# Optimization experiments

Hardware: AMD Instinct MI355X
Metric: run time of the kernel (lower is better)

## Reference

```python
import jax, jax.numpy as jnp
import numpy as np

NUM_BRANCHES = 3
NUM_LAYERS = 4
HIDDEN = 256
IN_DIM = 128
NUM_GRAPHS = 256
NUM_CLASSES = 10
TOPK_RATIO = 0.5
GATE_INIT = 0.8


def matrix_neighbors(branch, layer, num_branches):
    nbrs = []
    if layer > 0:
        nbrs.append((branch, layer - 1))
    for other in (branch - 1, branch + 1):
        if 0 <= other < num_branches:
            nbrs.append((other, layer))
    if layer > 0:
        for other in (branch - 1, branch + 1):
            if 0 <= other < num_branches:
                nbrs.append((other, layer - 1))
    return nbrs


def topk_mask(t, ratio):
    d = t.shape[-1]
    k = max(1, min(d, int(np.ceil(d * ratio))))
    if k >= d:
        return jnp.ones_like(t)
    _, idx = jax.lax.top_k(jnp.abs(t), k)
    rows = jnp.arange(t.shape[0])[:, None]
    return jnp.zeros_like(t).at[rows, idx].set(1.0)


def setup_inputs():
    key = jax.random.key(0)
    ks = jax.random.split(key, 10)
    n, e = 50000, 800000
    x = jax.random.normal(ks[0], (n, IN_DIM), dtype=jnp.float32)
    edge_index = jax.random.randint(ks[1], (2, e), 0, n)
    batch = jnp.sort(jax.random.randint(ks[2], (n,), 0, NUM_GRAPHS))
    s = 0.05
    Win = jax.random.normal(ks[3], (NUM_BRANCHES, IN_DIM, HIDDEN), dtype=jnp.float32) * s
    b_in = jnp.zeros((NUM_BRANCHES, HIDDEN), dtype=jnp.float32)
    Whid = jax.random.normal(ks[4], (NUM_LAYERS - 1, NUM_BRANCHES, HIDDEN, HIDDEN), dtype=jnp.float32) * s
    bhid = jnp.zeros((NUM_LAYERS - 1, NUM_BRANCHES, HIDDEN), dtype=jnp.float32)
    gate_logit = jnp.asarray(np.log(GATE_INIT / (1.0 - GATE_INIT)), dtype=jnp.float32)
    Wc = jax.random.normal(ks[5], (HIDDEN, NUM_CLASSES), dtype=jnp.float32) * s
    bc = jnp.zeros((NUM_CLASSES,), dtype=jnp.float32)
    return {"x": x, "edge_index": edge_index, "batch": batch, "Win": Win,
            "b_in": b_in, "Whid": Whid, "bhid": bhid, "gate_logit": gate_logit,
            "Wc": Wc, "bc": bc}


def _forward(x, edge_index, batch, Win, b_in, Whid, bhid, gate_logit, Wc, bc):
    n = x.shape[0]
    loops = jnp.arange(n)
    row = jnp.concatenate([edge_index[0], loops])  # source
    col = jnp.concatenate([edge_index[1], loops])  # target
    deg = jax.ops.segment_sum(jnp.ones_like(col, dtype=x.dtype), col, num_segments=n)
    dinv = jnp.where(deg > 0, jax.lax.rsqrt(deg), 0.0)
    norm = dinv[row] * dinv[col]  # [E+N]

    def gcn(h, W, b):
        hw = h @ W  # [n, H]
        agg = jax.ops.segment_sum(hw[row] * norm[:, None], col, num_segments=n)
        return agg + b

    gate = jax.nn.sigmoid(gate_logit)
    states = [x for _ in range(NUM_BRANCHES)]
    for layer in range(NUM_LAYERS):
        props = []
        for b in range(NUM_BRANCHES):
            if layer == 0:
                p = gcn(states[b], Win[b], b_in[b])
            else:
                p = gcn(states[b], Whid[layer - 1, b], bhid[layer - 1, b])
            props.append(jax.nn.relu(p))
        new_states = []
        for b in range(NUM_BRANCHES):
            fused = props[b]
            nbrs = matrix_neighbors(b, layer, NUM_BRANCHES)
            if nbrs:
                rs = jnp.zeros_like(fused)
                for (sb, sl) in nbrs:
                    src = props[sb] if sl == layer else states[sb]
                    rs = rs + src * topk_mask(src, TOPK_RATIO)
                fused = fused + gate * rs
            new_states.append(jax.nn.relu(fused))  # dropout is identity in eval
        states = new_states

    counts = jax.ops.segment_sum(jnp.ones((n,), dtype=x.dtype), batch, num_segments=NUM_GRAPHS)
    denom = jnp.maximum(counts, 1.0)[:, None]
    embs = [jax.ops.segment_sum(s, batch, num_segments=NUM_GRAPHS) / denom for s in states]
    final = jnp.mean(jnp.stack(embs, axis=0), axis=0)  # [G, H]
    logits = final @ Wc + bc
    return logits, final


def reference(x, edge_index, batch, Win, b_in, Whid, bhid, gate_logit, Wc, bc):
    return _forward(x, edge_index, batch, Win, b_in, Whid, bhid, gate_logit, Wc, bc)
```

## Files before the change

### kernel.cpp

```cpp
#include <hip/hip_runtime.h>
#include <hip/hip_fp16.h>

#define NB 3
#define HIDDEN 256
#define INDIM 128
#define NGRAPH 256
#define NCLS 10
#define NMAX 50048
#define EMAX 800000

typedef unsigned short u16;
typedef unsigned long long ull;
typedef _Float16 f16_t;
typedef f16_t f16x8 __attribute__((ext_vector_type(8)));
typedef float f32x4 __attribute__((ext_vector_type(4)));

__device__ __align__(16) u16   g_states[(size_t)NB * NMAX * HIDDEN];
__device__ __align__(16) u16   g_props [(size_t)NB * NMAX * HIDDEN];
__device__ __align__(16) u16   g_agg3 [(size_t)NB * NMAX * HIDDEN];
__device__ __align__(16) u16   g_xh    [(size_t)NMAX * INDIM];
__device__ __align__(16) u16   g_whin [(size_t)NB * INDIM * HIDDEN];
__device__ __align__(16) u16   g_whid [(size_t)9 * HIDDEN * HIDDEN];
__device__ float g_fin   [NGRAPH * HIDDEN];
__device__ float g_dinv  [NMAX];
__device__ float g_ewts  [EMAX];
__device__ int   g_rowptr[NMAX + 1];
__device__ int   g_cidx  [EMAX];
__device__ int   g_cnt   [NMAX];
__device__ int   g_gs    [NGRAPH];
__device__ int   g_gc    [NGRAPH];

union HU { u16 u; __half h; };
__device__ __forceinline__ float h2f(u16 v) { HU x; x.u = v; return __half2float(x.h); }
__device__ __forceinline__ u16 f2h(float f) { HU x; x.h = __float2half_rn(f); return x.u; }
__device__ __forceinline__ float relu_f(float x) { return x > 0.f ? x : 0.f; }

__device__ __forceinline__ void fma8(float* acc, uint4 v, float w) {
    unsigned uu[4] = {v.x, v.y, v.z, v.w};
    #pragma unroll
    for (int q = 0; q < 4; ++q) {
        HU lo, hi; lo.u = (u16)(uu[q] & 0xFFFFu); hi.u = (u16)(uu[q] >> 16);
        acc[q * 2 + 0] += w * __half2float(lo.h);
        acc[q * 2 + 1] += w * __half2float(hi.h);
    }
}

__global__ void zero_cnt_k(int n) {
    int i = blockIdx.x * 256 + threadIdx.x;
    if (i < n) g_cnt[i] = 0;
}
__global__ void zero_gk() {
    int i = threadIdx.x;
    g_gs[i] = 0; g_gc[i] = 0;
}
__global__ void cvt_xh_k(const float* __restrict__ x, int cnt) {
    int i = blockIdx.x * 256 + threadIdx.x;
    if (i < cnt) g_xh[i] = f2h(x[i]);
}
__global__ void cvt_wt_k(const float* __restrict__ src, int which, int K, int total) {
    int i = blockIdx.x * 256 + threadIdx.x;
    if (i >= total) return;
    int kc = K * 256;
    int b = i / kc; int rem = i - b * kc;
    int k = rem >> 8; int c = rem & 255;
    u16* dst = which ? g_whid : g_whin;
    dst[(size_t)b * kc + (size_t)c * K + k] = f2h(src[i]);
}

__global__ void count_edges_k(const int* __restrict__ col, int E) {
    int i = blockIdx.x * 256 + threadIdx.x;
    if (i < E) atomicAdd(&g_cnt[col[i]], 1);
}
__global__ void dinv_k(int n) {
    int i = blockIdx.x * 256 + threadIdx.x;
    if (i < n) g_dinv[i] = rsqrtf((float)(g_cnt[i] + 1));
}
__global__ __launch_bounds__(1024) void scan_k(int n) {
    __shared__ int sm[1024];
    __shared__ int carry_s;
    int t = threadIdx.x;
    if (t == 0) carry_s = 0;
    __syncthreads();
    for (int base = 0; base < n; base += 1024) {
        int i = base + t;
        int v = (i < n) ? g_cnt[i] : 0;
        sm[t] = v;
        __syncthreads();
        for (int off = 1; off < 1024; off <<= 1) {
            int u = (t >= off) ? sm[t - off] : 0;
            __syncthreads();
            sm[t] += u;
            __syncthreads();
        }
        int incl = sm[t];
        int c0 = carry_s;
        if (i < n) g_rowptr[i] = c0 + incl - v;
        __syncthreads();
        if (t == 0) carry_s += sm[1023];
        __syncthreads();
    }
    if (t == 0) g_rowptr[n] = carry_s;
}
__global__ void fill_csr_k(const int* __restrict__ row, const int* __restrict__ col, int E) {
    int i = blockIdx.x * 256 + threadIdx.x;
    if (i >= E) return;
    int r = row[i], c = col[i];
    int pos = g_rowptr[c] + atomicAdd(&g_cnt[c], 1);
    g_cidx[pos] = r;
    g_ewts[pos] = g_dinv[r] * g_dinv[c];
}

__global__ __launch_bounds__(256) void agg256x3_k(int n) {
    int node = blockIdx.x * 4 + (threadIdx.x >> 6);
    if (node >= n) return;
    int lane = threadIdx.x & 63;
    int half = lane >> 5;
    int li   = lane & 31;
    size_t pstride = (size_t)n * 32;
    const uint4* Sv = (const uint4*)g_states;
    float acc0[8] = {0,0,0,0,0,0,0,0}, acc1[8] = {0,0,0,0,0,0,0,0}, acc2[8] = {0,0,0,0,0,0,0,0};
    int e0 = g_rowptr[node], deg = g_rowptr[node + 1] - e0;
    int m = deg + 1;
    int j = half;
    if (half == 0) {
        float di = g_dinv[node];
        float w0 = di * di;
        size_t base = (size_t)node * 32 + li;
        fma8(acc0, Sv[base], w0);
        fma8(acc1, Sv[base + pstride], w0);
        fma8(acc2, Sv[base + 2 * pstride], w0);
        j = 2;
    }
    #pragma unroll 2
    for (; j < m; j += 2) {
        int s = g_cidx[e0 + j - 1];
        float w = g_ewts[e0 + j - 1];
        size_t base = (size_t)s * 32 + li;
        uint4 v0 = Sv[base], v1 = Sv[base + pstride], v2 = Sv[base + 2 * pstride];
        fma8(acc0, v0, w); fma8(acc1, v1, w); fma8(acc2, v2, w);
    }
    #pragma unroll
    for (int q = 0; q < 8; ++q) {
        acc0[q] += __shfl_xor(acc0[q], 32);
        acc1[q] += __shfl_xor(acc1[q], 32);
        acc2[q] += __shfl_xor(acc2[q], 32);
    }
    if (half == 0) {
        size_t stA = (size_t)NMAX * 32;
        uint4* Av = (uint4*)g_agg3;
        uint4 o;
        unsigned* ou = (unsigned*)&o;
        #pragma unroll
        for (int q = 0; q < 4; ++q) ou[q] = (unsigned)f2h(acc0[q*2]) | ((unsigned)f2h(acc0[q*2+1]) << 16);
        Av[(size_t)node * 32 + li] = o;
        #pragma unroll
        for (int q = 0; q < 4; ++q) ou[q] = (unsigned)f2h(acc1[q*2]) | ((unsigned)f2h(acc1[q*2+1]) << 16);
        Av[(size_t)node * 32 + li + stA] = o;
        #pragma unroll
        for (int q = 0; q < 4; ++q) ou[q] = (unsigned)f2h(acc2[q*2]) | ((unsigned)f2h(acc2[q*2+1]) << 16);
        Av[(size_t)node * 32 + li + 2 * stA] = o;
    }
}

__global__ __launch_bounds__(256) void agg128_k(int n) {
    int node = blockIdx.x * 4 + (threadIdx.x >> 6);
    if (node >= n) return;
    int lane = threadIdx.x & 63;
    int grp = lane >> 4;
    int li  = lane & 15;
    const uint4* Xv = (const uint4*)g_xh;
    float acc[8] = {0,0,0,0,0,0,0,0};
    int e0 = g_rowptr[node], deg = g_rowptr[node + 1] - e0;
    int m = deg + 1;
    int j = grp;
    if (grp == 0) {
        float di = g_dinv[node];
        fma8(acc, Xv[(size_t)node * 16 + li], di * di);
        j = 4;
    }
    #pragma unroll 2
    for (; j < m; j += 4) {
        int s = g_cidx[e0 + j - 1];
        float w = g_ewts[e0 + j - 1];
        fma8(acc, Xv[(size_t)s * 16 + li], w);
    }
    #pragma unroll
    for (int q = 0; q < 8; ++q) {
        acc[q] += __shfl_xor(acc[q], 16);
        acc[q] += __shfl_xor(acc[q], 32);
    }
    if (grp == 0) {
        uint4 o; unsigned* ou = (unsigned*)&o;
        #pragma unroll
        for (int q = 0; q < 4; ++q) ou[q] = (unsigned)f2h(acc[q*2]) | ((unsigned)f2h(acc[q*2+1]) << 16);
        ((uint4*)g_agg3)[(size_t)node * 16 + li] = o;
    }
}

template<int K>
__global__ __launch_bounds__(256) void gemm_mfma_k(int wsel, size_t aStride,
        const float* __restrict__ bias0, int n) {
    int br = blockIdx.y;
    const f16_t* A  = (const f16_t*)g_agg3 + (size_t)br * aStride;
    const f16_t* Wt = (wsel < 0) ? (const f16_t*)g_whin + (size_t)br * K * 256
                                 : (const f16_t*)g_whid + (size_t)(wsel + br) * K * 256;
    const float* bias = bias0 + (size_t)br * 256;
    u16* C = g_props + (size_t)br * n * 256;
    int t = threadIdx.x, l = t & 63, w = t >> 6;
    int row0 = blockIdx.x * 64;
    int c0 = w * 64;
    int mrow = l & 15;
    int kg = (l >> 4) * 8;
    f32x4 acc[4][4];
    #pragma unroll
    for (int rt = 0; rt < 4; ++rt)
        #pragma unroll
        for (int ct = 0; ct < 4; ++ct) acc[rt][ct] = (f32x4){0.f, 0.f, 0.f, 0.f};

    for (int k0 = 0; k0 < K; k0 += 32) {
        f16x8 af[4], bf[4];
        #pragma unroll
        for (int rt = 0; rt < 4; ++rt) {
            int r = row0 + rt * 16 + mrow;
            af[rt] = *(const f16x8*)(A + (size_t)r * K + k0 + kg);
        }
        #pragma unroll
        for (int ct = 0; ct < 4; ++ct) {
            int c = c0 + ct * 16 + mrow;
            bf[ct] = *(const f16x8*)(Wt + (size_t)c * K + k0 + kg);
        }
        #pragma unroll
        for (int rt = 0; rt < 4; ++rt)
            #pragma unroll
            for (int ct = 0; ct < 4; ++ct)
                acc[rt][ct] = __builtin_amdgcn_mfma_f32_16x16x32_f16(af[rt], bf[ct], acc[rt][ct], 0, 0, 0);
    }
    int rb = (l >> 4) * 4;
    #pragma unroll
    for (int ct = 0; ct < 4; ++ct) {
        int c = c0 + ct * 16 + mrow;
        float bv = bias[c];
        #pragma unroll
        for (int rt = 0; rt < 4; ++rt) {
            #pragma unroll
            for (int q = 0; q < 4; ++q) {
                int r = row0 + rt * 16 + rb + q;
                if (r < n) C[(size_t)r * 256 + c] = f2h(relu_f(acc[rt][ct][q] + bv));
            }
        }
    }
}

template<int CNT>
__device__ __forceinline__ void topk_multi(const ushort4* hu, const float4* v, float4* out) {
    int lane = threadIdx.x & 63;
    unsigned lo[CNT], hi[CNT]; int cge[CNT];
    #pragma unroll
    for (int s = 0; s < CNT; ++s) { lo[s] = 0; hi[s] = 0x7BFF; cge[s] = 256; }
    for (int it = 0; it < 15; ++it) {
        #pragma unroll
        for (int s = 0; s < CNT; ++s) {
            unsigned mid = (lo[s] + hi[s] + 1) >> 1;
            int c = __popcll(__ballot(hu[s].x >= mid)) + __popcll(__ballot(hu[s].y >= mid))
                  + __popcll(__ballot(hu[s].z >= mid)) + __popcll(__ballot(hu[s].w >= mid));
            if (c >= 128) { lo[s] = mid; cge[s] = c; } else hi[s] = mid - 1;
        }
    }
    #pragma unroll
    for (int s = 0; s < CNT; ++s) {
        unsigned thr = lo[s];
        unsigned a0 = hu[s].x, a1 = hu[s].y, a2 = hu[s].z, a3 = hu[s].w;
        float4 r;
        if (cge[s] == 128) {
            r.x = (a0 >= thr) ? v[s].x : 0.f;
            r.y = (a1 >= thr) ? v[s].y : 0.f;
            r.z = (a2 >= thr) ? v[s].z : 0.f;
            r.w = (a3 >= thr) ? v[s].w : 0.f;
        } else {
            ull b0 = __ballot(a0 == thr), b1 = __ballot(a1 == thr);
            ull b2 = __ballot(a2 == thr), b3 = __ballot(a3 == thr);
            int cgt = __popcll(__ballot(a0 > thr)) + __popcll(__ballot(a1 > thr))
                    + __popcll(__ballot(a2 > thr)) + __popcll(__ballot(a3 > thr));
            int need = 128 - cgt;
            ull below = (lane == 0) ? 0ull : (~0ull >> (64 - lane));
            int base = __popcll(b0 & below) + __popcll(b1 & below)
                     + __popcll(b2 & below) + __popcll(b3 & below);
            int o0 = (int)((b0 >> lane) & 1), o1 = (int)((b1 >> lane) & 1), o2 = (int)((b2 >> lane) & 1);
            int p0 = base, p1 = base + o0, p2 = p1 + o1, p3 = p2 + o2;
            r.x = (a0 > thr || (a0 == thr && p0 < need)) ? v[s].x : 0.f;
            r.y = (a1 > thr || (a1 == thr && p1 < need)) ? v[s].y : 0.f;
            r.z = (a2 > thr || (a2 == thr && p2 < need)) ? v[s].z : 0.f;
            r.w = (a3 > thr || (a3 == thr && p3 < need)) ? v[s].w : 0.f;
        }
        out[s] = r;
    }
}

__device__ __forceinline__ float4 dec4(ushort4 h) {
    float4 r; r.x = h2f(h.x); r.y = h2f(h.y); r.z = h2f(h.z); r.w = h2f(h.w);
    return r;
}
__device__ __forceinline__ void st4h(u16* p, size_t off, float4 v) {
    ushort4 o; o.x = f2h(v.x); o.y = f2h(v.y); o.z = f2h(v.z); o.w = f2h(v.w);
    ((ushort4*)p)[off] = o;
}

__global__ __launch_bounds__(256) void fuse0_k(const float* __restrict__ gate_logit, int n) {
    int node = blockIdx.x * 4 + (threadIdx.x >> 6);
    if (node >= n) return;
    int lane = threadIdx.x & 63;
    size_t stride = (size_t)n * 64;
    size_t off = (size_t)node * 64 + lane;
    float g = 1.f / (1.f + expf(-gate_logit[0]));
    const ushort4* P = (const ushort4*)g_props;
    ushort4 hu[3]; float4 v[3], m[3];
    hu[0] = P[off]; hu[1] = P[off + stride]; hu[2] = P[off + 2 * stride];
    v[0] = dec4(hu[0]); v[1] = dec4(hu[1]); v[2] = dec4(hu[2]);
    topk_multi<3>(hu, v, m);
    float4 o0, o1, o2;
    o0.x = relu_f(v[0].x + g * m[1].x); o0.y = relu_f(v[0].y + g * m[1].y);
    o0.z = relu_f(v[0].z + g * m[1].z); o0.w = relu_f(v[0].w + g * m[1].w);
    o1.x = relu_f(v[1].x + g * (m[0].x + m[2].x)); o1.y = relu_f(v[1].y + g * (m[0].y + m[2].y));
    o1.z = relu_f(v[1].z + g * (m[0].z + m[2].z)); o1.w = relu_f(v[1].w + g * (m[0].w + m[2].w));
    o2.x = relu_f(v[2].x + g * m[1].x); o2.y = relu_f(v[2].y + g * m[1].y);
    o2.z = relu_f(v[2].z + g * m[1].z); o2.w = relu_f(v[2].w + g * m[1].w);
    st4h(g_states, off, o0); st4h(g_states, off + stride, o1); st4h(g_states, off + 2 * stride, o2);
}

__global__ __launch_bounds__(256) void fuse_k(const float* __restrict__ gate_logit, int n) {
    int node = blockIdx.x * 4 + (threadIdx.x >> 6);
    if (node >= n) return;
    int lane = threadIdx.x & 63;
    size_t stride = (size_t)n * 64;
    size_t off = (size_t)node * 64 + lane;
    float g = 1.f / (1.f + expf(-gate_logit[0]));
    const ushort4* P = (const ushort4*)g_props;
    const ushort4* S = (const ushort4*)g_states;
    ushort4 hu[6]; float4 v[6], m[6];
    hu[0] = P[off]; hu[1] = P[off + stride]; hu[2] = P[off + 2 * stride];
    hu[3] = S[off]; hu[4] = S[off + stride]; hu[5] = S[off + 2 * stride];
    #pragma unroll
    for (int s = 0; s < 6; ++s) v[s] = dec4(hu[s]);
    topk_multi<6>(hu, v, m);
    float4 o0, o1, o2;
    o0.x = relu_f(v[0].x + g * (m[3].x + m[1].x + m[4].x));
    o0.y = relu_f(v[0].y + g * (m[3].y + m[1].y + m[4].y));
    o0.z = relu_f(v[0].z + g * (m[3].z + m[1].z + m[4].z));
    o0.w = relu_f(v[0].w + g * (m[3].w + m[1].w + m[4].w));
    o1.x = relu_f(v[1].x + g * (m[4].x + m[0].x + m[3].x + m[2].x + m[5].x));
    o1.y = relu_f(v[1].y + g * (m[4].y + m[0].y + m[3].y + m[2].y + m[5].y));
    o1.z = relu_f(v[1].z + g * (m[4].z + m[0].z + m[3].z + m[2].z + m[5].z));
    o1.w = relu_f(v[1].w + g * (m[4].w + m[0].w + m[3].w + m[2].w + m[5].w));
    o2.x = relu_f(v[2].x + g * (m[5].x + m[1].x + m[4].x));
    o2.y = relu_f(v[2].y + g * (m[5].y + m[1].y + m[4].y));
    o2.z = relu_f(v[2].z + g * (m[5].z + m[1].z + m[4].z));
    o2.w = relu_f(v[2].w + g * (m[5].w + m[1].w + m[4].w));
    st4h(g_states, off, o0); st4h(g_states, off + stride, o1); st4h(g_states, off + 2 * stride, o2);
}

__global__ void gbounds_k(const int* __restrict__ batch, int n) {
    int i = blockIdx.x * 256 + threadIdx.x;
    if (i >= n) return;
    int g = batch[i];
    atomicAdd(&g_gc[g], 1);
    if (i == 0 || batch[i - 1] != g) g_gs[g] = i;
}

__global__ __launch_bounds__(256) void greduce_k(float* __restrict__ outfin, int n) {
    int g = blockIdx.x, d = threadIdx.x;
    size_t stride = (size_t)n * 256;
    int st = g_gs[g], c = g_gc[g];
    float a = 0.f;
    for (int i = st; i < st + c; ++i) {
        size_t o = (size_t)i * 256 + d;
        a += h2f(g_states[o]) + h2f(g_states[o + stride]) + h2f(g_states[o + 2 * stride]);
    }
    float r = a / (3.0f * (float)(c > 0 ? c : 1));
    g_fin[g * 256 + d] = r;
    outfin[(size_t)g * 256 + d] = r;
}

__global__ void logits_k(const float* __restrict__ Wc, const float* __restrict__ bc,
                         float* __restrict__ out) {
    int idx = blockIdx.x * 256 + threadIdx.x;
    if (idx >= NGRAPH * NCLS) return;
    int g = idx / NCLS, c = idx % NCLS;
    float s = bc[c];
    for (int k = 0; k < 256; ++k) s += g_fin[g * 256 + k] * Wc[k * NCLS + c];
    out[idx] = s;
}

extern "C" void kernel_launch(void* const* d_in, const int* in_sizes, int n_in,
                              void* d_out, int out_size, void* d_ws, size_t ws_size,
                              hipStream_t stream) {
    const float* x       = (const float*)d_in[0];
    const int*   eidx    = (const int*)d_in[1];
    const int*   batch   = (const int*)d_in[2];
    const float* Win     = (const float*)d_in[3];
    const float* b_in    = (const float*)d_in[4];
    const float* Whid    = (const float*)d_in[5];
    const float* bhid    = (const float*)d_in[6];
    const float* gate_l  = (const float*)d_in[7];
    const float* Wc      = (const float*)d_in[8];
    const float* bc      = (const float*)d_in[9];
    float* out = (float*)d_out;

    const int n = in_sizes[0] / INDIM;
    const int E = in_sizes[1] / 2;
    if (n > NMAX || E > EMAX) return;
    const int* erow = eidx;
    const int* ecol = eidx + E;

    float* outfin = out + NGRAPH * NCLS;

    const int TB = 256;
    dim3 b256(TB);
    int nblkN = (n + TB - 1) / TB;
    int eblk  = (E + TB - 1) / TB;
    int nblk4 = (n + 3) / 4;
    dim3 ggrid((n + 63) / 64, NB);

    zero_cnt_k<<<nblkN, b256, 0, stream>>>(n);
    cvt_xh_k<<<(n * INDIM + TB - 1) / TB, b256, 0, stream>>>(x, n * INDIM);
    cvt_wt_k<<<(NB * INDIM * HIDDEN + TB - 1) / TB, b256, 0, stream>>>(Win, 0, INDIM, NB * INDIM * HIDDEN);
    cvt_wt_k<<<(9 * HIDDEN * HIDDEN + TB - 1) / TB, b256, 0, stream>>>(Whid, 1, HIDDEN, 9 * HIDDEN * HIDDEN);
    count_edges_k<<<eblk, b256, 0, stream>>>(ecol, E);
    dinv_k<<<nblkN, b256, 0, stream>>>(n);
    scan_k<<<1, 1024, 0, stream>>>(n);
    zero_cnt_k<<<nblkN, b256, 0, stream>>>(n);
    fill_csr_k<<<eblk, b256, 0, stream>>>(erow, ecol, E);

    agg128_k<<<nblk4, b256, 0, stream>>>(n);
    gemm_mfma_k<INDIM><<<ggrid, b256, 0, stream>>>(-1, (size_t)0, b_in, n);
    fuse0_k<<<nblk4, b256, 0, stream>>>(gate_l, n);

    for (int l = 1; l < 4; ++l) {
        agg256x3_k<<<nblk4, b256, 0, stream>>>(n);
        gemm_mfma_k<HIDDEN><<<ggrid, b256, 0, stream>>>((l - 1) * NB, (size_t)NMAX * 256,
                bhid + (size_t)(l - 1) * NB * HIDDEN, n);
        fuse_k<<<nblk4, b256, 0, stream>>>(gate_l, n);
    }

    zero_gk<<<1, 256, 0, stream>>>();
    gbounds_k<<<nblkN, b256, 0, stream>>>(batch, n);
    greduce_k<<<NGRAPH, b256, 0, stream>>>(outfin, n);
    logits_k<<<(NGRAPH * NCLS + TB - 1) / TB, b256, 0, stream>>>(Wc, bc, out);
}
```

Measured before the change: 1.912 ms.

## Interleave branch states per node in node-major layout

```diff
diff --git a/kernel.cpp b/kernel.cpp
--- a/kernel.cpp
+++ b/kernel.cpp
@@ -15,9 +15,9 @@
 typedef f16_t f16x8 __attribute__((ext_vector_type(8)));
 typedef float f32x4 __attribute__((ext_vector_type(4)));
 
-__device__ __align__(16) u16   g_states[(size_t)NB * NMAX * HIDDEN];
-__device__ __align__(16) u16   g_props [(size_t)NB * NMAX * HIDDEN];
-__device__ __align__(16) u16   g_agg3 [(size_t)NB * NMAX * HIDDEN];
+__device__ __align__(16) u16   g_states[(size_t)NMAX * NB * HIDDEN];
+__device__ __align__(16) u16   g_props [(size_t)NMAX * NB * HIDDEN];
+__device__ __align__(16) u16   g_agg3 [(size_t)NMAX * NB * HIDDEN];
 __device__ __align__(16) u16   g_xh    [(size_t)NMAX * INDIM];
 __device__ __align__(16) u16   g_whin [(size_t)NB * INDIM * HIDDEN];
 __device__ __align__(16) u16   g_whid [(size_t)9 * HIDDEN * HIDDEN];
@@ -116,7 +116,6 @@
     int lane = threadIdx.x & 63;
     int half = lane >> 5;
     int li   = lane & 31;
-    size_t pstride = (size_t)n * 32;
     const uint4* Sv = (const uint4*)g_states;
     float acc0[8] = {0,0,0,0,0,0,0,0}, acc1[8] = {0,0,0,0,0,0,0,0}, acc2[8] = {0,0,0,0,0,0,0,0};
     int e0 = g_rowptr[node], deg = g_rowptr[node + 1] - e0;
@@ -125,18 +124,18 @@
     if (half == 0) {
         float di = g_dinv[node];
         float w0 = di * di;
-        size_t base = (size_t)node * 32 + li;
+        size_t base = (size_t)node * 96 + li;
         fma8(acc0, Sv[base], w0);
-        fma8(acc1, Sv[base + pstride], w0);
-        fma8(acc2, Sv[base + 2 * pstride], w0);
+        fma8(acc1, Sv[base + 32], w0);
+        fma8(acc2, Sv[base + 64], w0);
         j = 2;
     }
     #pragma unroll 2
     for (; j < m; j += 2) {
         int s = g_cidx[e0 + j - 1];
         float w = g_ewts[e0 + j - 1];
-        size_t base = (size_t)s * 32 + li;
-        uint4 v0 = Sv[base], v1 = Sv[base + pstride], v2 = Sv[base + 2 * pstride];
+        size_t base = (size_t)s * 96 + li;
+        uint4 v0 = Sv[base], v1 = Sv[base + 32], v2 = Sv[base + 64];
         fma8(acc0, v0, w); fma8(acc1, v1, w); fma8(acc2, v2, w);
     }
     #pragma unroll
@@ -146,19 +145,19 @@
         acc2[q] += __shfl_xor(acc2[q], 32);
     }
     if (half == 0) {
-        size_t stA = (size_t)NMAX * 32;
         uint4* Av = (uint4*)g_agg3;
+        size_t base = (size_t)node * 96 + li;
         uint4 o;
         unsigned* ou = (unsigned*)&o;
         #pragma unroll
         for (int q = 0; q < 4; ++q) ou[q] = (unsigned)f2h(acc0[q*2]) | ((unsigned)f2h(acc0[q*2+1]) << 16);
-        Av[(size_t)node * 32 + li] = o;
+        Av[base] = o;
         #pragma unroll
         for (int q = 0; q < 4; ++q) ou[q] = (unsigned)f2h(acc1[q*2]) | ((unsigned)f2h(acc1[q*2+1]) << 16);
-        Av[(size_t)node * 32 + li + stA] = o;
+        Av[base + 32] = o;
         #pragma unroll
         for (int q = 0; q < 4; ++q) ou[q] = (unsigned)f2h(acc2[q*2]) | ((unsigned)f2h(acc2[q*2+1]) << 16);
-        Av[(size_t)node * 32 + li + 2 * stA] = o;
+        Av[base + 64] = o;
     }
 }
 
@@ -198,14 +197,14 @@
 }
 
 template<int K>
-__global__ __launch_bounds__(256) void gemm_mfma_k(int wsel, size_t aStride,
+__global__ __launch_bounds__(256) void gemm_mfma_k(int wsel, int rowStride, int brMul,
         const float* __restrict__ bias0, int n) {
     int br = blockIdx.y;
-    const f16_t* A  = (const f16_t*)g_agg3 + (size_t)br * aStride;
+    const f16_t* A  = (const f16_t*)g_agg3 + (size_t)br * brMul;
     const f16_t* Wt = (wsel < 0) ? (const f16_t*)g_whin + (size_t)br * K * 256
                                  : (const f16_t*)g_whid + (size_t)(wsel + br) * K * 256;
     const float* bias = bias0 + (size_t)br * 256;
-    u16* C = g_props + (size_t)br * n * 256;
+    u16* C = g_props + (size_t)br * 256;
     int t = threadIdx.x, l = t & 63, w = t >> 6;
     int row0 = blockIdx.x * 64;
     int c0 = w * 64;
@@ -222,7 +221,7 @@
         #pragma unroll
         for (int rt = 0; rt < 4; ++rt) {
             int r = row0 + rt * 16 + mrow;
-            af[rt] = *(const f16x8*)(A + (size_t)r * K + k0 + kg);
+            af[rt] = *(const f16x8*)(A + (size_t)r * rowStride + k0 + kg);
         }
         #pragma unroll
         for (int ct = 0; ct < 4; ++ct) {
@@ -245,7 +244,7 @@
             #pragma unroll
             for (int q = 0; q < 4; ++q) {
                 int r = row0 + rt * 16 + rb + q;
-                if (r < n) C[(size_t)r * 256 + c] = f2h(relu_f(acc[rt][ct][q] + bv));
+                if (r < n) C[(size_t)r * 768 + c] = f2h(relu_f(acc[rt][ct][q] + bv));
             }
         }
     }
@@ -309,12 +308,11 @@
     int node = blockIdx.x * 4 + (threadIdx.x >> 6);
     if (node >= n) return;
     int lane = threadIdx.x & 63;
-    size_t stride = (size_t)n * 64;
-    size_t off = (size_t)node * 64 + lane;
+    size_t base4 = (size_t)node * 192 + lane;
     float g = 1.f / (1.f + expf(-gate_logit[0]));
     const ushort4* P = (const ushort4*)g_props;
     ushort4 hu[3]; float4 v[3], m[3];
-    hu[0] = P[off]; hu[1] = P[off + stride]; hu[2] = P[off + 2 * stride];
+    hu[0] = P[base4]; hu[1] = P[base4 + 64]; hu[2] = P[base4 + 128];
     v[0] = dec4(hu[0]); v[1] = dec4(hu[1]); v[2] = dec4(hu[2]);
     topk_multi<3>(hu, v, m);
     float4 o0, o1, o2;
@@ -324,21 +322,20 @@
     o1.z = relu_f(v[1].z + g * (m[0].z + m[2].z)); o1.w = relu_f(v[1].w + g * (m[0].w + m[2].w));
     o2.x = relu_f(v[2].x + g * m[1].x); o2.y = relu_f(v[2].y + g * m[1].y);
     o2.z = relu_f(v[2].z + g * m[1].z); o2.w = relu_f(v[2].w + g * m[1].w);
-    st4h(g_states, off, o0); st4h(g_states, off + stride, o1); st4h(g_states, off + 2 * stride, o2);
+    st4h(g_states, base4, o0); st4h(g_states, base4 + 64, o1); st4h(g_states, base4 + 128, o2);
 }
 
 __global__ __launch_bounds__(256) void fuse_k(const float* __restrict__ gate_logit, int n) {
     int node = blockIdx.x * 4 + (threadIdx.x >> 6);
     if (node >= n) return;
     int lane = threadIdx.x & 63;
-    size_t stride = (size_t)n * 64;
-    size_t off = (size_t)node * 64 + lane;
+    size_t base4 = (size_t)node * 192 + lane;
     float g = 1.f / (1.f + expf(-gate_logit[0]));
     const ushort4* P = (const ushort4*)g_props;
     const ushort4* S = (const ushort4*)g_states;
     ushort4 hu[6]; float4 v[6], m[6];
-    hu[0] = P[off]; hu[1] = P[off + stride]; hu[2] = P[off + 2 * stride];
-    hu[3] = S[off]; hu[4] = S[off + stride]; hu[5] = S[off + 2 * stride];
+    hu[0] = P[base4]; hu[1] = P[base4 + 64]; hu[2] = P[base4 + 128];
+    hu[3] = S[base4]; hu[4] = S[base4 + 64]; hu[5] = S[base4 + 128];
     #pragma unroll
     for (int s = 0; s < 6; ++s) v[s] = dec4(hu[s]);
     topk_multi<6>(hu, v, m);
@@ -355,7 +352,7 @@
     o2.y = relu_f(v[2].y + g * (m[5].y + m[1].y + m[4].y));
     o2.z = relu_f(v[2].z + g * (m[5].z + m[1].z + m[4].z));
     o2.w = relu_f(v[2].w + g * (m[5].w + m[1].w + m[4].w));
-    st4h(g_states, off, o0); st4h(g_states, off + stride, o1); st4h(g_states, off + 2 * stride, o2);
+    st4h(g_states, base4, o0); st4h(g_states, base4 + 64, o1); st4h(g_states, base4 + 128, o2);
 }
 
 __global__ void gbounds_k(const int* __restrict__ batch, int n) {
@@ -368,12 +365,11 @@
 
 __global__ __launch_bounds__(256) void greduce_k(float* __restrict__ outfin, int n) {
     int g = blockIdx.x, d = threadIdx.x;
-    size_t stride = (size_t)n * 256;
     int st = g_gs[g], c = g_gc[g];
     float a = 0.f;
     for (int i = st; i < st + c; ++i) {
-        size_t o = (size_t)i * 256 + d;
-        a += h2f(g_states[o]) + h2f(g_states[o + stride]) + h2f(g_states[o + 2 * stride]);
+        size_t o = (size_t)i * 768 + d;
+        a += h2f(g_states[o]) + h2f(g_states[o + 256]) + h2f(g_states[o + 512]);
     }
     float r = a / (3.0f * (float)(c > 0 ? c : 1));
     g_fin[g * 256 + d] = r;
@@ -431,12 +427,12 @@
     fill_csr_k<<<eblk, b256, 0, stream>>>(erow, ecol, E);
 
     agg128_k<<<nblk4, b256, 0, stream>>>(n);
-    gemm_mfma_k<INDIM><<<ggrid, b256, 0, stream>>>(-1, (size_t)0, b_in, n);
+    gemm_mfma_k<INDIM><<<ggrid, b256, 0, stream>>>(-1, INDIM, 0, b_in, n);
     fuse0_k<<<nblk4, b256, 0, stream>>>(gate_l, n);
 
     for (int l = 1; l < 4; ++l) {
         agg256x3_k<<<nblk4, b256, 0, stream>>>(n);
-        gemm_mfma_k<HIDDEN><<<ggrid, b256, 0, stream>>>((l - 1) * NB, (size_t)NMAX * 256,
+        gemm_mfma_k<HIDDEN><<<ggrid, b256, 0, stream>>>((l - 1) * NB, NB * HIDDEN, HIDDEN,
                 bhid + (size_t)(l - 1) * NB * HIDDEN, n);
         fuse_k<<<nblk4, b256, 0, stream>>>(gate_l, n);
     }
```

Measured after the change: 1.869 ms. 1.02x faster.
